# Performance work log

Hardware: AMD Instinct MI355X
Metric: run time of the kernel (lower is better)

The kernel has to match this reference:

```python
import jax, jax.numpy as jnp
import numpy as np

T, M = 64, 64
ROI, SPA, WORD, I3D = 2048, 4, 300, 1024
H, D = 512, 256  # so_hidden, so_out_dim (= rel_dim)
IN = ROI + SPA + WORD  # 2352


def _w(k, shape):
    return jax.random.normal(k, shape, dtype=jnp.float32) * 0.02


def setup_inputs() -> dict:
    key = jax.random.key(0)
    ks = jax.random.split(key, 32)
    inp = {
        "roi_feats": jax.random.normal(ks[0], (T, M, ROI), dtype=jnp.float32),
        "spatial": jax.random.uniform(ks[1], (T, M, SPA), dtype=jnp.float32),
        "i3d_feats": jax.random.normal(ks[2], (T, I3D), dtype=jnp.float32),
        "subj_emb": jax.random.normal(ks[3], (WORD,), dtype=jnp.float32),
        "obj_emb": jax.random.normal(ks[4], (WORD,), dtype=jnp.float32),
        "pred_emb": jax.random.normal(ks[5], (WORD,), dtype=jnp.float32),
        # subject / object encoders (torch Linear convention: W is (out,in))
        "subj_w1": _w(ks[6], (H, IN)), "subj_b1": _w(ks[7], (H,)),
        "subj_w2": _w(ks[8], (D, H)), "subj_b2": _w(ks[9], (D,)),
        "obj_w1": _w(ks[10], (H, IN)), "obj_b1": _w(ks[11], (H,)),
        "obj_w2": _w(ks[12], (D, H)), "obj_b2": _w(ks[13], (D,)),
        # fuse MLPs (in = 2*D)
        "fuse_s_w1": _w(ks[14], (H, 2 * D)), "fuse_s_b1": _w(ks[15], (H,)),
        "fuse_s_w2": _w(ks[16], (D, H)), "fuse_s_b2": _w(ks[17], (D,)),
        "fuse_o_w1": _w(ks[18], (H, 2 * D)), "fuse_o_b1": _w(ks[19], (H,)),
        "fuse_o_w2": _w(ks[20], (D, H)), "fuse_o_b2": _w(ks[21], (D,)),
        # relation projections + MLP
        "W_rs": _w(ks[22], (D, D)),
        "W_ro": _w(ks[23], (D, D)),
        "rel_w1": _w(ks[24], (H, D + WORD)), "rel_b1": _w(ks[25], (H,)),
        "rel_w2": _w(ks[26], (D, H)), "rel_b2": _w(ks[27], (D,)),
    }
    return inp


def _linear(x, W, b):
    return x @ W.T + b


def _mlp2(x, w1, b1, w2, b2):
    return _linear(jax.nn.relu(_linear(x, w1, b1)), w2, b2)


def reference(roi_feats, spatial, i3d_feats, subj_emb, obj_emb, pred_emb,
              subj_w1, subj_b1, subj_w2, subj_b2,
              obj_w1, obj_b1, obj_w2, obj_b2,
              fuse_s_w1, fuse_s_b1, fuse_s_w2, fuse_s_b2,
              fuse_o_w1, fuse_o_b1, fuse_o_w2, fuse_o_b2,
              W_rs, W_ro, rel_w1, rel_b1, rel_w2, rel_b2):
    Tn, Mn, _ = roi_feats.shape
    se = jnp.broadcast_to(subj_emb, (Tn, Mn, subj_emb.shape[-1]))
    oe = jnp.broadcast_to(obj_emb, (Tn, Mn, obj_emb.shape[-1]))
    # SubjectObjectEncoder: fc2(relu(fc1([roi; spa; word])))
    fs_base = _mlp2(jnp.concatenate([roi_feats, spatial, se], axis=-1),
                    subj_w1, subj_b1, subj_w2, subj_b2)  # (T,M,D)
    fo_base = _mlp2(jnp.concatenate([roi_feats, spatial, oe], axis=-1),
                    obj_w1, obj_b1, obj_w2, obj_b2)
    # use_gsa = use_lla = False -> fuse([base; base])
    fs = _mlp2(jnp.concatenate([fs_base, fs_base], axis=-1),
               fuse_s_w1, fuse_s_b1, fuse_s_w2, fuse_s_b2)
    fo = _mlp2(jnp.concatenate([fo_base, fo_base], axis=-1),
               fuse_o_w1, fuse_o_b1, fuse_o_w2, fuse_o_b2)
    # Eq. 15: pairwise diff + predicate word, then 2-layer MLP
    fs_proj = fs @ W_rs.T
    fo_proj = fo @ W_ro.T
    diff = fs_proj[:, :, None, :] - fo_proj[:, None, :, :]  # (T,M,M,D)
    # rel_fc1([diff; pred]) split into diff part + constant pred part
    Wd, Wp = rel_w1[:, :fs.shape[-1]], rel_w1[:, fs.shape[-1]:]
    h = jax.nn.relu(diff @ Wd.T + (pred_emb @ Wp.T + rel_b1))  # (T,M,M,H)
    return h @ rel_w2.T + rel_b2  # (T,M,M,D)
```

## Files before the change

kernel.cpp:

```cpp
#include <hip/hip_runtime.h>
#include <hip/hip_bf16.h>

typedef __attribute__((ext_vector_type(4))) float f32x4;
typedef __attribute__((ext_vector_type(8))) short s16x8;

__device__ __forceinline__ void async_lds16(const void* g, void* l) {
  __builtin_amdgcn_global_load_lds((const __attribute__((address_space(1))) void*)g,
                                   (__attribute__((address_space(3))) void*)l, 16, 0, 0);
}

__device__ __forceinline__ short f2bf(float x) {
  __hip_bfloat16 h = __float2bfloat16(x);
  short s;
  __builtin_memcpy(&s, &h, 2);
  return s;
}

template<bool RELU, bool OUT_BF16>
__global__ __launch_bounds__(256) void gemm_bt(
    const __hip_bfloat16* __restrict__ Ag, const __hip_bfloat16* __restrict__ Bg,
    const float* __restrict__ biasg, void* __restrict__ Cg,
    int lda, int ldb, int K, int ldc,
    int strideA, int strideB, int strideBias, long strideC)
{
  __shared__ __align__(16) short As[4096];
  __shared__ __align__(16) short Bs[4096];
  const int tid  = threadIdx.x;
  const int lane = tid & 63;
  const int wid  = tid >> 6;
  const int z    = blockIdx.z;
  const __hip_bfloat16* A = Ag + (long)z * strideA;
  const __hip_bfloat16* B = Bg + (long)z * strideB;
  const float* bias = biasg + (long)z * strideBias;
  const int row0 = blockIdx.y * 128;
  const int col0 = blockIdx.x * 128;

  const int srow = wid * 16 + (lane >> 2);
  const int scol = (lane & 3) * 8;

  f32x4 acc[4][4];
#pragma unroll
  for (int i = 0; i < 4; ++i)
#pragma unroll
    for (int j = 0; j < 4; ++j) acc[i][j] = (f32x4)(0.0f);

  const int rw = (wid & 1) * 64;
  const int cw = (wid >> 1) * 64;
  const int lm = lane & 15;
  const int kg = (lane >> 4) * 8;

  for (int ks = 0; ks < K; ks += 32) {
    __syncthreads();
#pragma unroll
    for (int is = 0; is < 2; ++is) {
      async_lds16(A + (long)(row0 + is * 64 + srow) * lda + ks + scol,
                  (char*)As + is * 4096 + wid * 1024);
      async_lds16(B + (long)(col0 + is * 64 + srow) * ldb + ks + scol,
                  (char*)Bs + is * 4096 + wid * 1024);
    }
    __syncthreads();
    s16x8 af[4], bf[4];
#pragma unroll
    for (int mt = 0; mt < 4; ++mt)
      af[mt] = *(const s16x8*)(As + (rw + mt * 16 + lm) * 32 + kg);
#pragma unroll
    for (int nt = 0; nt < 4; ++nt)
      bf[nt] = *(const s16x8*)(Bs + (cw + nt * 16 + lm) * 32 + kg);
#pragma unroll
    for (int mt = 0; mt < 4; ++mt)
#pragma unroll
      for (int nt = 0; nt < 4; ++nt)
        acc[mt][nt] = __builtin_amdgcn_mfma_f32_16x16x32_bf16(af[mt], bf[nt], acc[mt][nt], 0, 0, 0);
  }

  const int lr4 = (lane >> 4) * 4;
#pragma unroll
  for (int mt = 0; mt < 4; ++mt) {
#pragma unroll
    for (int nt = 0; nt < 4; ++nt) {
      const int col = col0 + cw + nt * 16 + lm;
      const float bv = bias[col];
#pragma unroll
      for (int r = 0; r < 4; ++r) {
        const int row = row0 + rw + mt * 16 + lr4 + r;
        float v = acc[mt][nt][r] + bv;
        if (RELU) v = fmaxf(v, 0.0f);
        if (OUT_BF16)
          ((__hip_bfloat16*)Cg)[(long)z * strideC + (long)row * ldc + col] = __float2bfloat16(v);
        else
          ((float*)Cg)[(long)z * strideC + (long)row * ldc + col] = v;
      }
    }
  }
}

__global__ __launch_bounds__(256) void rel_final(
    const float* __restrict__ AsBo, const __hip_bfloat16* __restrict__ W2b,
    const float* __restrict__ b2, float* __restrict__ out)
{
  __shared__ __align__(16) short Hs[4096];
  __shared__ __align__(16) short Ws[4096];
  const int tid  = threadIdx.x;
  const int lane = tid & 63;
  const int wid  = tid >> 6;
  const int n0 = blockIdx.x * 128;
  const int i0 = blockIdx.y * 2;
  const int t  = blockIdx.z;

  const float* Ap = AsBo + (long)(t * 64 + i0) * 512;
  const float* Bp = AsBo + 2097152 + (long)t * 64 * 512;

  const int grow = tid >> 1;
  const int gkc  = (tid & 1) * 16;
  const float* arow = Ap + (grow >> 6) * 512 + gkc;
  const float* brow = Bp + (grow & 63) * 512 + gkc;
  short* hdst = Hs + grow * 32 + gkc;

  const int srow = wid * 16 + (lane >> 2);
  const int scol = (lane & 3) * 8;

  f32x4 acc[4][4];
#pragma unroll
  for (int i = 0; i < 4; ++i)
#pragma unroll
    for (int j = 0; j < 4; ++j) acc[i][j] = (f32x4)(0.0f);

  const int rw = (wid & 1) * 64;
  const int cw = (wid >> 1) * 64;
  const int lm = lane & 15;
  const int kg = (lane >> 4) * 8;

  for (int ks = 0; ks < 512; ks += 32) {
    __syncthreads();
#pragma unroll
    for (int is = 0; is < 2; ++is)
      async_lds16(W2b + (long)(n0 + is * 64 + srow) * 512 + ks + scol,
                  (char*)Ws + is * 4096 + wid * 1024);
    f32x4 av[4], bv[4];
#pragma unroll
    for (int q = 0; q < 4; ++q) {
      av[q] = *(const f32x4*)(arow + ks + q * 4);
      bv[q] = *(const f32x4*)(brow + ks + q * 4);
    }
    union { s16x8 v; short s[8]; } p0, p1;
#pragma unroll
    for (int q = 0; q < 2; ++q)
#pragma unroll
      for (int e = 0; e < 4; ++e) {
        p0.s[q * 4 + e] = f2bf(fmaxf(av[q][e] - bv[q][e], 0.0f));
        p1.s[q * 4 + e] = f2bf(fmaxf(av[q + 2][e] - bv[q + 2][e], 0.0f));
      }
    *(s16x8*)hdst = p0.v;
    *(s16x8*)(hdst + 8) = p1.v;
    __syncthreads();
    s16x8 af[4], bf[4];
#pragma unroll
    for (int mt = 0; mt < 4; ++mt)
      af[mt] = *(const s16x8*)(Hs + (rw + mt * 16 + lm) * 32 + kg);
#pragma unroll
    for (int nt = 0; nt < 4; ++nt)
      bf[nt] = *(const s16x8*)(Ws + (cw + nt * 16 + lm) * 32 + kg);
#pragma unroll
    for (int mt = 0; mt < 4; ++mt)
#pragma unroll
      for (int nt = 0; nt < 4; ++nt)
        acc[mt][nt] = __builtin_amdgcn_mfma_f32_16x16x32_bf16(af[mt], bf[nt], acc[mt][nt], 0, 0, 0);
  }

  const int lr4 = (lane >> 4) * 4;
#pragma unroll
  for (int mt = 0; mt < 4; ++mt) {
#pragma unroll
    for (int nt = 0; nt < 4; ++nt) {
      const int col = n0 + cw + nt * 16 + lm;
      const float bv = b2[col];
#pragma unroll
      for (int r = 0; r < 4; ++r) {
        const int prow = rw + mt * 16 + lr4 + r;
        const int il = prow >> 6, j = prow & 63;
        out[(long)((t * 64 + i0 + il) * 64 + j) * 256 + col] = acc[mt][nt][r] + bv;
      }
    }
  }
}

__global__ void prep_kernel(
    const float* __restrict__ roi, const float* __restrict__ spatial,
    const float* __restrict__ subj_emb, const float* __restrict__ obj_emb,
    const float* __restrict__ pred_emb,
    const float* __restrict__ subj_w1, const float* __restrict__ subj_b1,
    const float* __restrict__ obj_w1, const float* __restrict__ obj_b1,
    const float* __restrict__ subj_w2, const float* __restrict__ subj_b2,
    const float* __restrict__ obj_w2, const float* __restrict__ obj_b2,
    const float* __restrict__ fs_w1, const float* __restrict__ fs_b1,
    const float* __restrict__ fs_w2, const float* __restrict__ fs_b2,
    const float* __restrict__ fo_w1, const float* __restrict__ fo_b1,
    const float* __restrict__ fo_w2, const float* __restrict__ fo_b2,
    const float* __restrict__ W_rs, const float* __restrict__ W_ro,
    const float* __restrict__ rel_w1, const float* __restrict__ rel_b1,
    const float* __restrict__ rel_w2,
    __hip_bfloat16* __restrict__ XP, __hip_bfloat16* __restrict__ W1P,
    float* __restrict__ cboth,
    __hip_bfloat16* __restrict__ Bcat2, float* __restrict__ bias2,
    __hip_bfloat16* __restrict__ WfCat, float* __restrict__ biasf,
    __hip_bfloat16* __restrict__ W4cat, float* __restrict__ bias4,
    __hip_bfloat16* __restrict__ WcCat, float* __restrict__ crel,
    __hip_bfloat16* __restrict__ W2b)
{
  long id = (long)blockIdx.x * blockDim.x + threadIdx.x;

  if (id < 8519680L) {
    int row = (int)(id / 2080), col = (int)(id % 2080);
    float v = 0.0f;
    if (col < 2048) v = roi[(long)row * 2048 + col];
    else if (col < 2052) v = spatial[row * 4 + (col - 2048)];
    XP[id] = __float2bfloat16(v);
    return;
  }
  id -= 8519680L;
  if (id < 2129920L) {
    int row = (int)(id / 2080), col = (int)(id % 2080);
    const float* w = (row < 512) ? (subj_w1 + (long)row * 2352)
                                 : (obj_w1 + (long)(row - 512) * 2352);
    float v = (col < 2052) ? w[col] : 0.0f;
    W1P[id] = __float2bfloat16(v);
    return;
  }
  id -= 2129920L;
  if (id < 1024) {
    int h = (int)id;
    const float* w; const float* e; float s;
    if (h < 512) { w = subj_w1 + (long)h * 2352 + 2052; e = subj_emb; s = subj_b1[h]; }
    else { w = obj_w1 + (long)(h - 512) * 2352 + 2052; e = obj_emb; s = obj_b1[h - 512]; }
    for (int k = 0; k < 300; ++k) s += w[k] * e[k];
    cboth[h] = s;
    return;
  }
  id -= 1024;
  if (id < 262144) {
    int z = (int)(id >> 17); int r = (int)(id & 131071);
    Bcat2[id] = __float2bfloat16((z ? obj_w2 : subj_w2)[r]);
    return;
  }
  id -= 262144;
  if (id < 512) { bias2[id] = (id < 256) ? subj_b2[id] : obj_b2[id - 256]; return; }
  id -= 512;
  if (id < 262144) {
    int z = (int)(id >> 17); int r = (int)(id & 131071);
    int h = r >> 8, d = r & 255;
    const float* w = z ? fo_w1 : fs_w1;
    WfCat[id] = __float2bfloat16(w[h * 512 + d] + w[h * 512 + 256 + d]);
    return;
  }
  id -= 262144;
  if (id < 1024) { biasf[id] = (id < 512) ? fs_b1[id] : fo_b1[id - 512]; return; }
  id -= 1024;
  if (id < 262144) {
    int z = (int)(id >> 17); int r = (int)(id & 131071);
    W4cat[id] = __float2bfloat16((z ? fo_w2 : fs_w2)[r]);
    return;
  }
  id -= 262144;
  if (id < 512) { bias4[id] = (id < 256) ? fs_b2[id] : fo_b2[id - 256]; return; }
  id -= 512;
  if (id < 262144) {
    int z = (int)(id >> 17); int r = (int)(id & 131071);
    int h = r >> 8, d = r & 255;
    const float* Wr = z ? W_ro : W_rs;
    const float* wd = rel_w1 + (long)h * 556;
    float s = 0.0f;
    for (int e = 0; e < 256; ++e) s += wd[e] * Wr[e * 256 + d];
    WcCat[id] = __float2bfloat16(s);
    return;
  }
  id -= 262144;
  if (id < 1024) {
    int z = (int)(id >> 9); int h = (int)(id & 511);
    float s = 0.0f;
    if (z == 0) {
      s = rel_b1[h];
      const float* wp = rel_w1 + (long)h * 556 + 256;
      for (int k = 0; k < 300; ++k) s += pred_emb[k] * wp[k];
    }
    crel[id] = s;
    return;
  }
  id -= 1024;
  if (id < 131072) { W2b[id] = __float2bfloat16(rel_w2[id]); return; }
}

extern "C" void kernel_launch(void* const* d_in, const int* in_sizes, int n_in,
                              void* d_out, int out_size, void* d_ws, size_t ws_size,
                              hipStream_t stream)
{
  const float* roi       = (const float*)d_in[0];
  const float* spatial   = (const float*)d_in[1];
  const float* subj_emb  = (const float*)d_in[3];
  const float* obj_emb   = (const float*)d_in[4];
  const float* pred_emb  = (const float*)d_in[5];
  const float* subj_w1   = (const float*)d_in[6];
  const float* subj_b1   = (const float*)d_in[7];
  const float* subj_w2   = (const float*)d_in[8];
  const float* subj_b2   = (const float*)d_in[9];
  const float* obj_w1    = (const float*)d_in[10];
  const float* obj_b1    = (const float*)d_in[11];
  const float* obj_w2    = (const float*)d_in[12];
  const float* obj_b2    = (const float*)d_in[13];
  const float* fuse_s_w1 = (const float*)d_in[14];
  const float* fuse_s_b1 = (const float*)d_in[15];
  const float* fuse_s_w2 = (const float*)d_in[16];
  const float* fuse_s_b2 = (const float*)d_in[17];
  const float* fuse_o_w1 = (const float*)d_in[18];
  const float* fuse_o_b1 = (const float*)d_in[19];
  const float* fuse_o_w2 = (const float*)d_in[20];
  const float* fuse_o_b2 = (const float*)d_in[21];
  const float* W_rs      = (const float*)d_in[22];
  const float* W_ro      = (const float*)d_in[23];
  const float* rel_w1    = (const float*)d_in[24];
  const float* rel_b1    = (const float*)d_in[25];
  const float* rel_w2    = (const float*)d_in[26];
  const float* rel_b2    = (const float*)d_in[27];

  char* ws = (char*)d_ws;
  __hip_bfloat16* XP   = (__hip_bfloat16*)(ws);
  float*          AsBo = (float*)(ws);
  __hip_bfloat16* W1P  = (__hip_bfloat16*)(ws + 17039360);
  __hip_bfloat16* H1   = (__hip_bfloat16*)(ws + 21299200);
  __hip_bfloat16* FS   = (__hip_bfloat16*)(ws + 29687808);
  const size_t so = 33882112;
  __hip_bfloat16* Bcat2 = (__hip_bfloat16*)(ws + so);
  float*          bias2 = (float*)(ws + so + 524288);
  __hip_bfloat16* WfCat = (__hip_bfloat16*)(ws + so + 526336);
  float*          biasf = (float*)(ws + so + 1050624);
  __hip_bfloat16* W4cat = (__hip_bfloat16*)(ws + so + 1054720);
  float*          bias4 = (float*)(ws + so + 1579008);
  __hip_bfloat16* WcCat = (__hip_bfloat16*)(ws + so + 1581056);
  float*          crel  = (float*)(ws + so + 2105344);
  __hip_bfloat16* W2b   = (__hip_bfloat16*)(ws + so + 2109440);
  float*          cboth = (float*)(ws + so + 2371584);

  prep_kernel<<<46224, 256, 0, stream>>>(
      roi, spatial, subj_emb, obj_emb, pred_emb,
      subj_w1, subj_b1, obj_w1, obj_b1, subj_w2, subj_b2, obj_w2, obj_b2,
      fuse_s_w1, fuse_s_b1, fuse_s_w2, fuse_s_b2,
      fuse_o_w1, fuse_o_b1, fuse_o_w2, fuse_o_b2,
      W_rs, W_ro, rel_w1, rel_b1, rel_w2,
      XP, W1P, cboth, Bcat2, bias2, WfCat, biasf, W4cat, bias4, WcCat, crel, W2b);

  gemm_bt<true, true><<<dim3(8, 32, 1), 256, 0, stream>>>(
      XP, W1P, cboth, H1, 2080, 2080, 2080, 1024, 0, 0, 0, 0);
  gemm_bt<false, true><<<dim3(2, 32, 2), 256, 0, stream>>>(
      H1, Bcat2, bias2, FS, 1024, 512, 512, 512, 512, 131072, 256, 256);
  gemm_bt<true, true><<<dim3(4, 32, 2), 256, 0, stream>>>(
      FS, WfCat, biasf, H1, 512, 256, 256, 1024, 256, 131072, 512, 512);
  gemm_bt<false, true><<<dim3(2, 32, 2), 256, 0, stream>>>(
      H1, W4cat, bias4, FS, 1024, 512, 512, 512, 512, 131072, 256, 256);
  gemm_bt<false, false><<<dim3(4, 32, 2), 256, 0, stream>>>(
      FS, WcCat, crel, AsBo, 512, 256, 256, 512, 256, 131072, 512, 2097152L);
  rel_final<<<dim3(2, 32, 64), 256, 0, stream>>>(AsBo, W2b, rel_b2, (float*)d_out);
}
```

Before: 615.7 us.

## Split-K first GEMM, use 64x64 tiles for small GEMMs, vectorize prep

The first encoder GEMM (K≈2080) is split into two K halves, each writing fp32 partials, and a new reduce kernel adds them with the bias, applies ReLU and packs to bf16. This doubles the block count for the long-K GEMM. The four smaller GEMMs move to a 64x64-tile variant so more workgroups fill the GPU. The prep kernel now converts eight floats per thread with vector loads and packed bf16 stores, and padding grows to 2112 columns. The cost is an extra fp32 partial buffer round-trip and one more launch.

```diff
diff --git a/kernel.cpp b/kernel.cpp
--- a/kernel.cpp
+++ b/kernel.cpp
@@ -16,7 +16,14 @@
   return s;
 }
 
-template<bool RELU, bool OUT_BF16>
+__device__ __forceinline__ s16x8 pack8(f32x4 a, f32x4 b) {
+  s16x8 r;
+  r[0] = f2bf(a[0]); r[1] = f2bf(a[1]); r[2] = f2bf(a[2]); r[3] = f2bf(a[3]);
+  r[4] = f2bf(b[0]); r[5] = f2bf(b[1]); r[6] = f2bf(b[2]); r[7] = f2bf(b[3]);
+  return r;
+}
+
+template<bool RELU, bool OUT_BF16, bool HAS_BIAS>
 __global__ __launch_bounds__(256) void gemm_bt(
     const __hip_bfloat16* __restrict__ Ag, const __hip_bfloat16* __restrict__ Bg,
     const float* __restrict__ biasg, void* __restrict__ Cg,
@@ -31,7 +38,7 @@
   const int z    = blockIdx.z;
   const __hip_bfloat16* A = Ag + (long)z * strideA;
   const __hip_bfloat16* B = Bg + (long)z * strideB;
-  const float* bias = biasg + (long)z * strideBias;
+  const float* bias = HAS_BIAS ? (biasg + (long)z * strideBias) : nullptr;
   const int row0 = blockIdx.y * 128;
   const int col0 = blockIdx.x * 128;
 
@@ -79,7 +86,7 @@
 #pragma unroll
     for (int nt = 0; nt < 4; ++nt) {
       const int col = col0 + cw + nt * 16 + lm;
-      const float bv = bias[col];
+      const float bv = HAS_BIAS ? bias[col] : 0.0f;
 #pragma unroll
       for (int r = 0; r < 4; ++r) {
         const int row = row0 + rw + mt * 16 + lr4 + r;
@@ -94,6 +101,95 @@
   }
 }
 
+template<bool RELU, bool OUT_BF16, bool HAS_BIAS>
+__global__ __launch_bounds__(256) void gemm_bt64(
+    const __hip_bfloat16* __restrict__ Ag, const __hip_bfloat16* __restrict__ Bg,
+    const float* __restrict__ biasg, void* __restrict__ Cg,
+    int lda, int ldb, int K, int ldc,
+    int strideA, int strideB, int strideBias, long strideC)
+{
+  __shared__ __align__(16) short As[2048];
+  __shared__ __align__(16) short Bs[2048];
+  const int tid  = threadIdx.x;
+  const int lane = tid & 63;
+  const int wid  = tid >> 6;
+  const int z    = blockIdx.z;
+  const __hip_bfloat16* A = Ag + (long)z * strideA;
+  const __hip_bfloat16* B = Bg + (long)z * strideB;
+  const float* bias = HAS_BIAS ? (biasg + (long)z * strideBias) : nullptr;
+  const int row0 = blockIdx.y * 64;
+  const int col0 = blockIdx.x * 64;
+
+  const int srow = wid * 16 + (lane >> 2);
+  const int scol = (lane & 3) * 8;
+
+  f32x4 acc[2][2];
+#pragma unroll
+  for (int i = 0; i < 2; ++i)
+#pragma unroll
+    for (int j = 0; j < 2; ++j) acc[i][j] = (f32x4)(0.0f);
+
+  const int rw = (wid & 1) * 32;
+  const int cw = (wid >> 1) * 32;
+  const int lm = lane & 15;
+  const int kg = (lane >> 4) * 8;
+
+  for (int ks = 0; ks < K; ks += 32) {
+    __syncthreads();
+    async_lds16(A + (long)(row0 + srow) * lda + ks + scol, (char*)As + wid * 1024);
+    async_lds16(B + (long)(col0 + srow) * ldb + ks + scol, (char*)Bs + wid * 1024);
+    __syncthreads();
+    s16x8 af[2], bf[2];
+#pragma unroll
+    for (int mt = 0; mt < 2; ++mt)
+      af[mt] = *(const s16x8*)(As + (rw + mt * 16 + lm) * 32 + kg);
+#pragma unroll
+    for (int nt = 0; nt < 2; ++nt)
+      bf[nt] = *(const s16x8*)(Bs + (cw + nt * 16 + lm) * 32 + kg);
+#pragma unroll
+    for (int mt = 0; mt < 2; ++mt)
+#pragma unroll
+      for (int nt = 0; nt < 2; ++nt)
+        acc[mt][nt] = __builtin_amdgcn_mfma_f32_16x16x32_bf16(af[mt], bf[nt], acc[mt][nt], 0, 0, 0);
+  }
+
+  const int lr4 = (lane >> 4) * 4;
+#pragma unroll
+  for (int mt = 0; mt < 2; ++mt) {
+#pragma unroll
+    for (int nt = 0; nt < 2; ++nt) {
+      const int col = col0 + cw + nt * 16 + lm;
+      const float bv = HAS_BIAS ? bias[col] : 0.0f;
+#pragma unroll
+      for (int r = 0; r < 4; ++r) {
+        const int row = row0 + rw + mt * 16 + lr4 + r;
+        float v = acc[mt][nt][r] + bv;
+        if (RELU) v = fmaxf(v, 0.0f);
+        if (OUT_BF16)
+          ((__hip_bfloat16*)Cg)[(long)z * strideC + (long)row * ldc + col] = __float2bfloat16(v);
+        else
+          ((float*)Cg)[(long)z * strideC + (long)row * ldc + col] = v;
+      }
+    }
+  }
+}
+
+__global__ __launch_bounds__(256) void reduce_relu(
+    const float* __restrict__ P, const float* __restrict__ cboth,
+    __hip_bfloat16* __restrict__ H1)
+{
+  const int id = blockIdx.x * 256 + threadIdx.x;
+  const int row = id >> 7, c8 = id & 127;
+  const f32x4* p0 = (const f32x4*)(P + (long)row * 1024 + c8 * 8);
+  const f32x4* p1 = (const f32x4*)(P + 4194304 + (long)row * 1024 + c8 * 8);
+  const f32x4* bb = (const f32x4*)(cboth + c8 * 8);
+  f32x4 a = p0[0] + p1[0] + bb[0];
+  f32x4 b = p0[1] + p1[1] + bb[1];
+#pragma unroll
+  for (int e = 0; e < 4; ++e) { a[e] = fmaxf(a[e], 0.0f); b[e] = fmaxf(b[e], 0.0f); }
+  *(s16x8*)((short*)H1 + (long)row * 1024 + c8 * 8) = pack8(a, b);
+}
+
 __global__ __launch_bounds__(256) void rel_final(
     const float* __restrict__ AsBo, const __hip_bfloat16* __restrict__ W2b,
     const float* __restrict__ b2, float* __restrict__ out)
@@ -184,7 +280,7 @@
   }
 }
 
-__global__ void prep_kernel(
+__global__ __launch_bounds__(256) void prep_kernel(
     const float* __restrict__ roi, const float* __restrict__ spatial,
     const float* __restrict__ subj_emb, const float* __restrict__ obj_emb,
     const float* __restrict__ pred_emb,
@@ -207,28 +303,54 @@
     __hip_bfloat16* __restrict__ WcCat, float* __restrict__ crel,
     __hip_bfloat16* __restrict__ W2b)
 {
-  long id = (long)blockIdx.x * blockDim.x + threadIdx.x;
-
-  if (id < 8519680L) {
-    int row = (int)(id / 2080), col = (int)(id % 2080);
-    float v = 0.0f;
-    if (col < 2048) v = roi[(long)row * 2048 + col];
-    else if (col < 2052) v = spatial[row * 4 + (col - 2048)];
-    XP[id] = __float2bfloat16(v);
-    return;
-  }
-  id -= 8519680L;
-  if (id < 2129920L) {
-    int row = (int)(id / 2080), col = (int)(id % 2080);
+  int id = blockIdx.x * 256 + threadIdx.x;
+
+  if (id < 1081344) {
+    int row = id / 264, c8 = id - row * 264;
+    s16x8 o;
+    if (c8 < 256) {
+      const f32x4* src = (const f32x4*)(roi + (long)row * 2048 + c8 * 8);
+      o = pack8(src[0], src[1]);
+    } else {
+      f32x4 a, b;
+#pragma unroll
+      for (int e = 0; e < 4; ++e) {
+        int col = c8 * 8 + e;
+        a[e] = (col < 2052) ? spatial[row * 4 + (col - 2048)] : 0.0f;
+        int col2 = col + 4;
+        b[e] = (col2 < 2052) ? spatial[row * 4 + (col2 - 2048)] : 0.0f;
+      }
+      o = pack8(a, b);
+    }
+    *(s16x8*)((short*)XP + (long)id * 8) = o;
+    return;
+  }
+  id -= 1081344;
+  if (id < 270336) {
+    int row = id / 264, c8 = id - row * 264;
     const float* w = (row < 512) ? (subj_w1 + (long)row * 2352)
                                  : (obj_w1 + (long)(row - 512) * 2352);
-    float v = (col < 2052) ? w[col] : 0.0f;
-    W1P[id] = __float2bfloat16(v);
-    return;
-  }
-  id -= 2129920L;
+    s16x8 o;
+    if (c8 < 256) {
+      const f32x4* src = (const f32x4*)(w + c8 * 8);
+      o = pack8(src[0], src[1]);
+    } else {
+      f32x4 a, b;
+#pragma unroll
+      for (int e = 0; e < 4; ++e) {
+        int col = c8 * 8 + e;
+        a[e] = (col < 2052) ? w[col] : 0.0f;
+        int col2 = col + 4;
+        b[e] = (col2 < 2052) ? w[col2] : 0.0f;
+      }
+      o = pack8(a, b);
+    }
+    *(s16x8*)((short*)W1P + (long)id * 8) = o;
+    return;
+  }
+  id -= 270336;
   if (id < 1024) {
-    int h = (int)id;
+    int h = id;
     const float* w; const float* e; float s;
     if (h < 512) { w = subj_w1 + (long)h * 2352 + 2052; e = subj_emb; s = subj_b1[h]; }
     else { w = obj_w1 + (long)(h - 512) * 2352 + 2052; e = obj_emb; s = obj_b1[h - 512]; }
@@ -237,34 +359,38 @@
     return;
   }
   id -= 1024;
-  if (id < 262144) {
-    int z = (int)(id >> 17); int r = (int)(id & 131071);
-    Bcat2[id] = __float2bfloat16((z ? obj_w2 : subj_w2)[r]);
-    return;
-  }
-  id -= 262144;
+  if (id < 32768) {
+    const float* src = (id < 16384) ? (subj_w2 + id * 8) : (obj_w2 + (id - 16384) * 8);
+    const f32x4* s4 = (const f32x4*)src;
+    *(s16x8*)((short*)Bcat2 + (long)id * 8) = pack8(s4[0], s4[1]);
+    return;
+  }
+  id -= 32768;
   if (id < 512) { bias2[id] = (id < 256) ? subj_b2[id] : obj_b2[id - 256]; return; }
   id -= 512;
-  if (id < 262144) {
-    int z = (int)(id >> 17); int r = (int)(id & 131071);
-    int h = r >> 8, d = r & 255;
-    const float* w = z ? fo_w1 : fs_w1;
-    WfCat[id] = __float2bfloat16(w[h * 512 + d] + w[h * 512 + 256 + d]);
-    return;
-  }
-  id -= 262144;
+  if (id < 32768) {
+    int z = id >> 14, r8 = id & 16383;
+    int h = r8 >> 5, d8 = r8 & 31;
+    const float* w = (z ? fo_w1 : fs_w1) + h * 512 + d8 * 8;
+    const f32x4* lo = (const f32x4*)w;
+    const f32x4* hi = (const f32x4*)(w + 256);
+    *(s16x8*)((short*)WfCat + (long)id * 8) = pack8(lo[0] + hi[0], lo[1] + hi[1]);
+    return;
+  }
+  id -= 32768;
   if (id < 1024) { biasf[id] = (id < 512) ? fs_b1[id] : fo_b1[id - 512]; return; }
   id -= 1024;
-  if (id < 262144) {
-    int z = (int)(id >> 17); int r = (int)(id & 131071);
-    W4cat[id] = __float2bfloat16((z ? fo_w2 : fs_w2)[r]);
-    return;
-  }
-  id -= 262144;
+  if (id < 32768) {
+    const float* src = (id < 16384) ? (fs_w2 + id * 8) : (fo_w2 + (id - 16384) * 8);
+    const f32x4* s4 = (const f32x4*)src;
+    *(s16x8*)((short*)W4cat + (long)id * 8) = pack8(s4[0], s4[1]);
+    return;
+  }
+  id -= 32768;
   if (id < 512) { bias4[id] = (id < 256) ? fs_b2[id] : fo_b2[id - 256]; return; }
   id -= 512;
   if (id < 262144) {
-    int z = (int)(id >> 17); int r = (int)(id & 131071);
+    int z = id >> 17, r = id & 131071;
     int h = r >> 8, d = r & 255;
     const float* Wr = z ? W_ro : W_rs;
     const float* wd = rel_w1 + (long)h * 556;
@@ -275,7 +401,7 @@
   }
   id -= 262144;
   if (id < 1024) {
-    int z = (int)(id >> 9); int h = (int)(id & 511);
+    int z = id >> 9, h = id & 511;
     float s = 0.0f;
     if (z == 0) {
       s = rel_b1[h];
@@ -286,7 +412,10 @@
     return;
   }
   id -= 1024;
-  if (id < 131072) { W2b[id] = __float2bfloat16(rel_w2[id]); return; }
+  if (id < 16384) {
+    const f32x4* s4 = (const f32x4*)(rel_w2 + id * 8);
+    *(s16x8*)((short*)W2b + (long)id * 8) = pack8(s4[0], s4[1]);
+  }
 }
 
 extern "C" void kernel_launch(void* const* d_in, const int* in_sizes, int n_in,
@@ -324,10 +453,11 @@
   char* ws = (char*)d_ws;
   __hip_bfloat16* XP   = (__hip_bfloat16*)(ws);
   float*          AsBo = (float*)(ws);
-  __hip_bfloat16* W1P  = (__hip_bfloat16*)(ws + 17039360);
-  __hip_bfloat16* H1   = (__hip_bfloat16*)(ws + 21299200);
-  __hip_bfloat16* FS   = (__hip_bfloat16*)(ws + 29687808);
-  const size_t so = 33882112;
+  __hip_bfloat16* W1P  = (__hip_bfloat16*)(ws + 17301504);
+  __hip_bfloat16* H1   = (__hip_bfloat16*)(ws + 21626880);
+  __hip_bfloat16* FS   = (__hip_bfloat16*)(ws + 30015488);
+  float*          P    = (float*)(ws + 34209792);
+  const size_t so = 67764224;
   __hip_bfloat16* Bcat2 = (__hip_bfloat16*)(ws + so);
   float*          bias2 = (float*)(ws + so + 524288);
   __hip_bfloat16* WfCat = (__hip_bfloat16*)(ws + so + 526336);
@@ -339,7 +469,7 @@
   __hip_bfloat16* W2b   = (__hip_bfloat16*)(ws + so + 2109440);
   float*          cboth = (float*)(ws + so + 2371584);
 
-  prep_kernel<<<46224, 256, 0, stream>>>(
+  prep_kernel<<<6768, 256, 0, stream>>>(
       roi, spatial, subj_emb, obj_emb, pred_emb,
       subj_w1, subj_b1, obj_w1, obj_b1, subj_w2, subj_b2, obj_w2, obj_b2,
       fuse_s_w1, fuse_s_b1, fuse_s_w2, fuse_s_b2,
@@ -347,15 +477,16 @@
       W_rs, W_ro, rel_w1, rel_b1, rel_w2,
       XP, W1P, cboth, Bcat2, bias2, WfCat, biasf, W4cat, bias4, WcCat, crel, W2b);
 
-  gemm_bt<true, true><<<dim3(8, 32, 1), 256, 0, stream>>>(
-      XP, W1P, cboth, H1, 2080, 2080, 2080, 1024, 0, 0, 0, 0);
-  gemm_bt<false, true><<<dim3(2, 32, 2), 256, 0, stream>>>(
+  gemm_bt<false, false, false><<<dim3(8, 32, 2), 256, 0, stream>>>(
+      XP, W1P, cboth, P, 2112, 2112, 1056, 1024, 1056, 1056, 0, 4194304L);
+  reduce_relu<<<2048, 256, 0, stream>>>(P, cboth, H1);
+  gemm_bt64<false, true, true><<<dim3(4, 64, 2), 256, 0, stream>>>(
       H1, Bcat2, bias2, FS, 1024, 512, 512, 512, 512, 131072, 256, 256);
-  gemm_bt<true, true><<<dim3(4, 32, 2), 256, 0, stream>>>(
+  gemm_bt64<true, true, true><<<dim3(8, 64, 2), 256, 0, stream>>>(
       FS, WfCat, biasf, H1, 512, 256, 256, 1024, 256, 131072, 512, 512);
-  gemm_bt<false, true><<<dim3(2, 32, 2), 256, 0, stream>>>(
+  gemm_bt64<false, true, true><<<dim3(4, 64, 2), 256, 0, stream>>>(
       H1, W4cat, bias4, FS, 1024, 512, 512, 512, 512, 131072, 256, 256);
-  gemm_bt<false, false><<<dim3(4, 32, 2), 256, 0, stream>>>(
+  gemm_bt64<false, false, true><<<dim3(8, 64, 2), 256, 0, stream>>>(
       FS, WcCat, crel, AsBo, 512, 256, 256, 512, 256, 131072, 512, 2097152L);
   rel_final<<<dim3(2, 32, 64), 256, 0, stream>>>(AsBo, W2b, rel_b2, (float*)d_out);
 }
```

Result: faster. 574.5 us (-6.7%).
